# Kernel optimization log

Measured on AMD Instinct MI355X. Metric: run time of the kernel, lower is better.

The kernel has to match this reference:

```python
import jax, jax.numpy as jnp
import numpy as np

NEG = -1e30


def setup_inputs() -> dict:
    B, Lc, Lq, D = 64, 2048, 256, 128
    key = jax.random.key(0)
    kC, kQ, kcm, kqm, k1, k2, k3 = jax.random.split(key, 7)
    C = jax.random.normal(kC, (B, Lc, D), dtype=jnp.float32)
    Q = jax.random.normal(kQ, (B, Lq, D), dtype=jnp.float32)
    Cmask = jax.random.randint(kcm, (B, Lc), 0, 2).astype(jnp.float32)
    Qmask = jax.random.randint(kqm, (B, Lq), 0, 2).astype(jnp.float32)
    # xavier_uniform for (D,1): bound = sqrt(6/(D+1))
    b1 = float(np.sqrt(6.0 / (D + 1)))
    w4C = jax.random.uniform(k1, (D, 1), minval=-b1, maxval=b1, dtype=jnp.float32)
    w4Q = jax.random.uniform(k2, (D, 1), minval=-b1, maxval=b1, dtype=jnp.float32)
    # xavier_uniform for (1,1,D): fan_in=D, fan_out=1 on last two dims -> bound = sqrt(6/(1+D))
    w4mlu = jax.random.uniform(k3, (1, 1, D), minval=-b1, maxval=b1, dtype=jnp.float32)
    bias = jnp.zeros((1,), dtype=jnp.float32)
    return {"C": C, "Q": Q, "Cmask": Cmask, "Qmask": Qmask,
            "w4C": w4C, "w4Q": w4Q, "w4mlu": w4mlu, "bias": bias}


def reference(C, Q, Cmask, Qmask, w4C, w4Q, w4mlu, bias):
    # trilinear score S: [B, Lc, Lq]  (eval mode: dropout is identity)
    sub0 = C @ w4C                                   # [B, Lc, 1]
    sub1 = jnp.transpose(Q @ w4Q, (0, 2, 1))         # [B, 1, Lq]
    sub2 = jnp.einsum('bcd,bqd->bcq', C * w4mlu, Q)  # [B, Lc, Lq]
    S = sub0 + sub1 + sub2 + bias
    Qm = Qmask[:, None, :]   # [B, 1, Lq]
    Cm = Cmask[:, :, None]   # [B, Lc, 1]
    S1 = jax.nn.softmax(S + NEG * (1.0 - Qm), axis=2)  # over query
    S2 = jax.nn.softmax(S + NEG * (1.0 - Cm), axis=1)  # over context
    A = jnp.einsum('bcq,bqd->bcd', S1, Q)              # [B, Lc, D]
    Bt = jnp.einsum('bcq,bkq,bkd->bcd', S1, S2, C)     # S1 @ S2^T @ C
    out = jnp.concatenate([C, A, C * A, C * Bt], axis=2)  # [B, Lc, 4D]
    return jnp.transpose(out, (0, 2, 1))               # [B, 4D, Lc]
```

## Files before the change

### kernel.cpp

```cpp
#include <hip/hip_runtime.h>

#define B_ 64
#define LC 2048
#define LQ 256
#define DD 128

typedef __bf16 bf16;
typedef __bf16 bf16x8 __attribute__((ext_vector_type(8)));
typedef __bf16 bf16x4 __attribute__((ext_vector_type(4)));
typedef float f32x4 __attribute__((ext_vector_type(4)));

#define MFMA16(a, b, c) __builtin_amdgcn_mfma_f32_16x16x32_bf16((a), (b), (c), 0, 0, 0)


__global__ __launch_bounds__(256) void k_prep(const float* __restrict__ C,
    const float* __restrict__ Q, const float* __restrict__ w4C,
    const float* __restrict__ w4Q, const float* __restrict__ w4mlu,
    bf16* __restrict__ Cwp, bf16* __restrict__ CbTp,
    bf16* __restrict__ Qbp, bf16* __restrict__ QbTp,
    float* __restrict__ sub0, float* __restrict__ sub1, float* __restrict__ out)
{
    __shared__ float lds[64][DD + 4];
    int t = threadIdx.x;
    if (blockIdx.x < 2048) {
        int b = blockIdx.x >> 5, ct = blockIdx.x & 31;
        int c0 = ct * 64;
        int r = t >> 2, cb = (t & 3) * 32;
        size_t rowoff = ((size_t)(b * LC + c0 + r)) * DD + cb;
        const float4* src = (const float4*)(C + rowoff);
        float s0 = 0.f;
#pragma unroll
        for (int i = 0; i < 8; ++i) {
            float4 v = src[i];
            int d = cb + i * 4;
            lds[r][d] = v.x; lds[r][d + 1] = v.y; lds[r][d + 2] = v.z; lds[r][d + 3] = v.w;
            s0 += v.x * w4C[d] + v.y * w4C[d + 1] + v.z * w4C[d + 2] + v.w * w4C[d + 3];
        }
        s0 += __shfl_xor(s0, 1);
        s0 += __shfl_xor(s0, 2);
        if ((t & 3) == 0) sub0[b * LC + c0 + r] = s0;
        __syncthreads();

#pragma unroll
        for (int p = 0; p < 4; ++p) {
            int idx = p * 256 + t;
            int chunk = idx >> 6, w = idx & 63;
            int cb_l = chunk >> 2, ks = chunk & 3;
            int lr = w & 15, lg = w >> 4;
            int c_l = cb_l * 16 + lr, d0 = ks * 32 + lg * 8;
            bf16x8 v;
#pragma unroll
            for (int j = 0; j < 8; ++j) v[j] = (bf16)(lds[c_l][d0 + j] * w4mlu[d0 + j]);
            size_t off = ((size_t)((b * 128 + ct * 4 + cb_l) * 4 + ks)) * 512 + w * 8;
            *(bf16x8*)(Cwp + off) = v;
        }
#pragma unroll
        for (int p = 0; p < 4; ++p) {
            int idx = p * 256 + t;
            int cb32 = idx >> 9, rem = idx & 511;
            int d = rem >> 2, lg = rem & 3;
            int cl0 = cb32 * 32 + lg * 8;
            bf16x8 v;
#pragma unroll
            for (int j = 0; j < 8; ++j) v[j] = (bf16)lds[cl0 + j][d];
            size_t off = ((size_t)((b * 64 + ct * 2 + cb32) * 128 + d)) * 32 + lg * 8;
            *(bf16x8*)(CbTp + off) = v;
        }
#pragma unroll
        for (int p = 0; p < 8; ++p) {
            int d = p * 16 + (t >> 4);
            int cl = (t & 15) * 4;
            f32x4 v = {lds[cl][d], lds[cl + 1][d], lds[cl + 2][d], lds[cl + 3][d]};
            __builtin_nontemporal_store(v,
                (f32x4*)(out + ((size_t)(b * 512 + d)) * LC + c0 + cl));
        }
    } else {
        int idx0 = blockIdx.x - 2048;
        int b = idx0 >> 2, qt = idx0 & 3;
        int q0 = qt * 64;
        bf16* ldsb = (bf16*)lds;
        int r = t >> 2, cb = (t & 3) * 32;
        size_t rowoff = ((size_t)(b * LQ + q0 + r)) * DD + cb;
        const float4* src = (const float4*)(Q + rowoff);
        float s1 = 0.f;
#pragma unroll
        for (int i = 0; i < 8; ++i) {
            float4 v = src[i];
            int d = cb + i * 4;
            ldsb[r * 132 + d] = (bf16)v.x; ldsb[r * 132 + d + 1] = (bf16)v.y;
            ldsb[r * 132 + d + 2] = (bf16)v.z; ldsb[r * 132 + d + 3] = (bf16)v.w;
            s1 += v.x * w4Q[d] + v.y * w4Q[d + 1] + v.z * w4Q[d + 2] + v.w * w4Q[d + 3];
        }
        s1 += __shfl_xor(s1, 1);
        s1 += __shfl_xor(s1, 2);
        if ((t & 3) == 0) sub1[b * LQ + q0 + r] = s1;
        __syncthreads();

#pragma unroll
        for (int p = 0; p < 4; ++p) {
            int idx = p * 256 + t;
            int chunk = idx >> 6, w = idx & 63;
            int qb_l = chunk >> 2, ks = chunk & 3;
            int lr = w & 15, lg = w >> 4;
            bf16x8 v = *(bf16x8*)&ldsb[(qb_l * 16 + lr) * 132 + ks * 32 + lg * 8];
            size_t off = ((size_t)((b * 16 + qt * 4 + qb_l) * 4 + ks)) * 512 + w * 8;
            *(bf16x8*)(Qbp + off) = v;
        }
#pragma unroll
        for (int p = 0; p < 4; ++p) {
            int idx = p * 256 + t;
            int chunk = idx >> 6, w = idx & 63;
            int ks_l = chunk >> 3, dt = chunk & 7;
            int lr = w & 15, lg = w >> 4;
            int d = dt * 16 + lr, ql = ks_l * 32 + lg * 8;
            bf16x8 v;
#pragma unroll
            for (int j = 0; j < 8; ++j) v[j] = ldsb[(ql + j) * 132 + d];
            size_t off = ((size_t)((b * 8 + qt * 2 + ks_l) * 8 + dt)) * 512 + w * 8;
            *(bf16x8*)(QbTp + off) = v;
        }
    }
}

__global__ __launch_bounds__(256) void k_s(const bf16* __restrict__ Cwp,
    const bf16* __restrict__ Qbp, const float* __restrict__ sub0,
    const float* __restrict__ sub1, const float* __restrict__ Qmask,
    const float* __restrict__ Cmask, const float* __restrict__ bias,
    bf16* __restrict__ Pp, float* __restrict__ Rpart, float* __restrict__ Lpart)
{
    __shared__ bf16 ldsP[128][82];
    int id = blockIdx.x;
    int xcd = id & 7, slot = id >> 3;
    int b = xcd * 8 + (slot >> 6);
    int rem = slot & 63;
    int ctile = rem >> 2, qt = rem & 3;
    int q0 = qt * 64;
    int t = threadIdx.x, wid = t >> 6, lane = t & 63;
    int lr = lane & 15, lg = lane >> 4;
    int rowbase = ctile * 128 + wid * 32;

    f32x4 acc[2][4];
#pragma unroll
    for (int rt = 0; rt < 2; ++rt)
#pragma unroll
        for (int ct = 0; ct < 4; ++ct) acc[rt][ct] = (f32x4){0.f, 0.f, 0.f, 0.f};

    const bf16* Ab = Cwp + ((size_t)((b * 128 + ctile * 8 + wid * 2) * 4)) * 512 + lane * 8;
    const bf16* Bb = Qbp + ((size_t)((b * 16 + qt * 4) * 4)) * 512 + lane * 8;
#pragma unroll
    for (int ks = 0; ks < 4; ++ks) {
        bf16x8 a0 = *(const bf16x8*)(Ab + (size_t)ks * 512);
        bf16x8 a1 = *(const bf16x8*)(Ab + (size_t)(4 + ks) * 512);
#pragma unroll
        for (int ct = 0; ct < 4; ++ct) {
            bf16x8 bb = *(const bf16x8*)(Bb + (size_t)(ct * 4 + ks) * 512);
            acc[0][ct] = MFMA16(a0, bb, acc[0][ct]);
            acc[1][ct] = MFMA16(a1, bb, acc[1][ct]);
        }
    }

    float biasv = bias[0];
    float sub0v[2][4], cmv[2][4];
#pragma unroll
    for (int rt = 0; rt < 2; ++rt)
#pragma unroll
        for (int j = 0; j < 4; ++j) {
            int idx = b * LC + rowbase + rt * 16 + lg * 4 + j;
            sub0v[rt][j] = sub0[idx];
            cmv[rt][j] = Cmask[idx];
        }

    float rsum[2][4] = {};
#pragma unroll
    for (int ct = 0; ct < 4; ++ct) {
        int q = q0 + ct * 16 + lr;
        float s1v = sub1[b * LQ + q] + biasv;
        float qm = Qmask[b * LQ + q];
        float colsum = 0.f;
#pragma unroll
        for (int rt = 0; rt < 2; ++rt)
#pragma unroll
            for (int j = 0; j < 4; ++j) {
                float S = acc[rt][ct][j] + sub0v[rt][j] + s1v;
                float Pv = __expf(S - 8.0f) * qm;
                rsum[rt][j] += Pv;
                colsum += Pv * cmv[rt][j];
                ldsP[wid * 32 + rt * 16 + lg * 4 + j][ct * 16 + lr] = (bf16)Pv;
            }
        colsum += __shfl_xor(colsum, 16);
        colsum += __shfl_xor(colsum, 32);
        if (lg == 0)
            Lpart[((size_t)(b * 64 + ctile * 4 + wid)) * LQ + q] = colsum;
    }
#pragma unroll
    for (int rt = 0; rt < 2; ++rt)
#pragma unroll
        for (int j = 0; j < 4; ++j) {
            float s = rsum[rt][j];
            s += __shfl_xor(s, 1);
            s += __shfl_xor(s, 2);
            s += __shfl_xor(s, 4);
            s += __shfl_xor(s, 8);
            if (lr == 0)
                Rpart[((size_t)(b * 4 + qt)) * LC + rowbase + rt * 16 + lg * 4 + j] = s;
        }
    __syncthreads();

#pragma unroll
    for (int p = 0; p < 4; ++p) {
        int idx = p * 256 + t;
        int chunk = idx >> 6, w = idx & 63;
        int cb_l = chunk >> 1, ks_l = chunk & 1;
        int plr = w & 15, plg = w >> 4;
        bf16x8 v = *(bf16x8*)&ldsP[cb_l * 16 + plr][ks_l * 32 + plg * 8];
        size_t off = ((size_t)((b * 128 + ctile * 8 + cb_l) * 8 + qt * 2 + ks_l)) * 512 + w * 8;
        *(bf16x8*)(Pp + off) = v;
    }
}

__global__ __launch_bounds__(256) void k_m(const bf16* __restrict__ CbTp,
    const bf16* __restrict__ Pp, const float* __restrict__ Cmask,
    bf16* __restrict__ MTp)
{
    __shared__ bf16 stage[2][64 * 40];
    int id = blockIdx.x;
    int xcd = id & 7, slot = id >> 3;
    int b = xcd * 8 + (slot >> 4);
    int rem = slot & 15;
    int qt = rem & 3, ksl = rem >> 2;
    int t = threadIdx.x, wid = t >> 6, lane = t & 63;
    int lr = lane & 15, lg = lane >> 4;
    int dbase = wid * 32;

    f32x4 acc[2][4];
#pragma unroll
    for (int rt = 0; rt < 2; ++rt)
#pragma unroll
        for (int ct = 0; ct < 4; ++ct) acc[rt][ct] = (f32x4){0.f, 0.f, 0.f, 0.f};

    const bf16* Ab = CbTp + ((size_t)(b * 64 + ksl * 16) * 128 + dbase + lr) * 32 + lg * 8;
    const float* Mb = Cmask + b * LC + ksl * 512 + lg * 8;
    int cb_off = wid & 1, qh = wid >> 1;
    const bf16* Bsrc = Pp + ((size_t)((b * 128 + ksl * 32 + cb_off) * 8) + qt * 2 + qh) * 512
                       + lane * 8;
    int c_local = cb_off * 16 + lr;
    int qrow = qh * 32 + lg * 8;

    {
        bf16x8 g = *(const bf16x8*)Bsrc;
#pragma unroll
        for (int i = 0; i < 8; ++i) stage[0][(qrow + i) * 40 + c_local] = g[i];
    }
    __syncthreads();

    for (int ks = 0; ks < 16; ++ks) {
        int cur = ks & 1;
        bf16x8 g;
        if (ks < 15) g = *(const bf16x8*)(Bsrc + (size_t)(ks + 1) * 8192);
        bf16x8 a0 = *(const bf16x8*)(Ab + (size_t)ks * 4096);
        bf16x8 a1 = *(const bf16x8*)(Ab + (size_t)ks * 4096 + 512);
        f32x4 m0 = *(const f32x4*)(Mb + ks * 32);
        f32x4 m1 = *(const f32x4*)(Mb + ks * 32 + 4);
        bf16x8 msk;
#pragma unroll
        for (int i = 0; i < 4; ++i) { msk[i] = (bf16)m0[i]; msk[4 + i] = (bf16)m1[i]; }
        a0 = a0 * msk;
        a1 = a1 * msk;
#pragma unroll
        for (int ct = 0; ct < 4; ++ct) {
            bf16x8 bb = *(bf16x8*)&stage[cur][(ct * 16 + lr) * 40 + lg * 8];
            acc[0][ct] = MFMA16(a0, bb, acc[0][ct]);
            acc[1][ct] = MFMA16(a1, bb, acc[1][ct]);
        }
        if (ks < 15) {
#pragma unroll
            for (int i = 0; i < 8; ++i) stage[cur ^ 1][(qrow + i) * 40 + c_local] = g[i];
        }
        __syncthreads();
    }

    size_t base = ((((size_t)ksl * B_ + b) * 4 + qt) * 4 + wid) * 2048;
#pragma unroll
    for (int rt = 0; rt < 2; ++rt)
#pragma unroll
        for (int ct = 0; ct < 4; ++ct)
#pragma unroll
            for (int j = 0; j < 4; ++j)
                MTp[base + (size_t)(rt * 16 + ct * 4 + j) * 64 + lane] = (bf16)acc[rt][ct][j];
}

__global__ __launch_bounds__(256) void k_m2(const bf16* __restrict__ MTp,
    const float* __restrict__ Lpart, bf16* __restrict__ MTpn)
{
    __shared__ float ldsLinv[256];
    int b = blockIdx.y, ih = blockIdx.x;
    int t = threadIdx.x;
    {
        float s = 0.f;
#pragma unroll
        for (int sl = 0; sl < 64; ++sl) s += Lpart[((size_t)(b * 64 + sl)) * LQ + t];
        ldsLinv[t] = 1.0f / fmaxf(s, 1e-30f);
    }
    __syncthreads();
#pragma unroll
    for (int i = 0; i < 4; ++i) {
        int slot = (ih * 4 + i) * 256 + t;
        int d = slot >> 5, qo = slot & 31;
        int q0 = qo * 8;
        int qt = q0 >> 6, ct = (q0 >> 4) & 3, lr0 = q0 & 15;
        int wid = d >> 5, rt = (d >> 4) & 1, lgd = (d >> 2) & 3, j = d & 3;
        size_t roff = ((size_t)(b * 4 + qt)) * 8192 + wid * 2048
                      + (rt * 16 + ct * 4 + j) * 64 + lgd * 16 + lr0;
        float a8[8] = {0.f, 0.f, 0.f, 0.f, 0.f, 0.f, 0.f, 0.f};
#pragma unroll
        for (int sl = 0; sl < 4; ++sl) {
            bf16x8 x = *(const bf16x8*)(MTp + (size_t)sl * B_ * 32768 + roff);
#pragma unroll
            for (int k = 0; k < 8; ++k) a8[k] += (float)x[k];
        }
        bf16x8 o;
#pragma unroll
        for (int k = 0; k < 8; ++k) o[k] = (bf16)(a8[k] * ldsLinv[q0 + k]);
        size_t woff = ((size_t)((b * 8 + (qo >> 2)) * 8 + (d >> 4))) * 512
                      + ((qo & 3) * 16 + (d & 15)) * 8;
        *(bf16x8*)(MTpn + woff) = o;
    }
}

__global__ __launch_bounds__(256) void k_out(const bf16* __restrict__ Pp,
    const bf16* __restrict__ QbTp, const bf16* __restrict__ MTpn,
    const bf16* __restrict__ CbTp, const float* __restrict__ Rpart,
    float* __restrict__ out)
{
    __shared__ f32x4 smem4[2304];
    bf16* stage = (bf16*)smem4;
    bf16 (*ldsA)[72] = (bf16(*)[72])smem4;
    bf16 (*ldsB)[72] = (bf16(*)[72])((char*)smem4 + 18432);

    int id = blockIdx.x;
    int xcd = id & 7, slot = id >> 3;
    int b = xcd * 8 + (slot >> 5);
    int ctile = slot & 31;
    int t = threadIdx.x, wid = t >> 6, lane = t & 63;
    int lr = lane & 15, lg = lane >> 4;
    int c0 = ctile * 64;

    const bf16* gsrc = (wid < 2 ? QbTp : MTpn) + (size_t)b * 32768
                       + (size_t)(wid & 1) * 2048 + lane * 8;
    int ldst = wid * 2048 + lane * 8;

    f32x4 rs = (f32x4){0.f, 0.f, 0.f, 0.f};
#pragma unroll
    for (int s = 0; s < 4; ++s)
        rs += *(const f32x4*)(Rpart + ((size_t)(b * 4 + s)) * LC + c0 + wid * 16 + lg * 4);
    f32x4 rv;
#pragma unroll
    for (int j = 0; j < 4; ++j) rv[j] = 1.0f / fmaxf(rs[j], 1e-30f);

    f32x4 accA[8], accB[8];
#pragma unroll
    for (int dt = 0; dt < 8; ++dt) {
        accA[dt] = (f32x4){0.f, 0.f, 0.f, 0.f};
        accB[dt] = (f32x4){0.f, 0.f, 0.f, 0.f};
    }
    const bf16* Ab = Pp + ((size_t)((b * 128 + ctile * 4 + wid) * 8)) * 512 + lane * 8;

    {
        bf16x8 g0 = *(const bf16x8*)(gsrc);
        bf16x8 g1 = *(const bf16x8*)(gsrc + 512);
        bf16x8 g2 = *(const bf16x8*)(gsrc + 1024);
        bf16x8 g3 = *(const bf16x8*)(gsrc + 1536);
        *(bf16x8*)&stage[ldst]        = g0;
        *(bf16x8*)&stage[ldst + 512]  = g1;
        *(bf16x8*)&stage[ldst + 1024] = g2;
        *(bf16x8*)&stage[ldst + 1536] = g3;
    }
    __syncthreads();

    for (int ks = 0; ks < 8; ++ks) {
        int cur = (ks & 1) * 8192;
        bf16x8 g0, g1, g2, g3;
        if (ks < 7) {
            const bf16* gs = gsrc + (size_t)(ks + 1) * 4096;
            g0 = *(const bf16x8*)(gs);
            g1 = *(const bf16x8*)(gs + 512);
            g2 = *(const bf16x8*)(gs + 1024);
            g3 = *(const bf16x8*)(gs + 1536);
        }
        bf16x8 a = *(const bf16x8*)(Ab + (size_t)ks * 512);
        int foff = cur + lane * 8;
#pragma unroll
        for (int dt = 0; dt < 8; ++dt) {
            bf16x8 bq = *(bf16x8*)&stage[foff + dt * 512];
            bf16x8 bm = *(bf16x8*)&stage[foff + 4096 + dt * 512];
            accA[dt] = MFMA16(a, bq, accA[dt]);
            accB[dt] = MFMA16(a, bm, accB[dt]);
        }
        if (ks < 7) {
            int nb = cur ^ 8192;
            *(bf16x8*)&stage[nb + ldst]        = g0;
            *(bf16x8*)&stage[nb + ldst + 512]  = g1;
            *(bf16x8*)&stage[nb + ldst + 1024] = g2;
            *(bf16x8*)&stage[nb + ldst + 1536] = g3;
        }
        __syncthreads();
    }

    int fsub = t >> 4;
    int cq = (t & 15) * 4;
    int cglob = c0 + cq;
    int cb32g = cglob >> 5, cig = cglob & 31;
    bf16x4 cpre[8];
#pragma unroll
    for (int pass = 0; pass < 8; ++pass) {
        int d = pass * 16 + fsub;
        cpre[pass] = *(const bf16x4*)(CbTp + ((size_t)(b * 64 + cb32g) * 128 + d) * 32 + cig);
    }

#pragma unroll
    for (int dt = 0; dt < 8; ++dt) {
        f32x4 a4 = accA[dt] * rv;
        f32x4 b4 = accB[dt] * rv;
        bf16x4 pa = { (bf16)a4[0], (bf16)a4[1], (bf16)a4[2], (bf16)a4[3] };
        bf16x4 pb = { (bf16)b4[0], (bf16)b4[1], (bf16)b4[2], (bf16)b4[3] };
        *(bf16x4*)&ldsA[dt * 16 + lr][wid * 16 + lg * 4] = pa;
        *(bf16x4*)&ldsB[dt * 16 + lr][wid * 16 + lg * 4] = pb;
    }
    __syncthreads();

    float* obase = out + ((size_t)b * 512) * LC;
#pragma unroll
    for (int pass = 0; pass < 8; ++pass) {
        int d = pass * 16 + fsub;
        bf16x4 av = *(bf16x4*)&ldsA[d][cq];
        bf16x4 bv = *(bf16x4*)&ldsB[d][cq];
        bf16x4 cb4 = cpre[pass];
        f32x4 c4 = {(float)cb4[0], (float)cb4[1], (float)cb4[2], (float)cb4[3]};
        f32x4 a4 = {(float)av[0], (float)av[1], (float)av[2], (float)av[3]};
        f32x4 b4 = {(float)bv[0], (float)bv[1], (float)bv[2], (float)bv[3]};
        __builtin_nontemporal_store(a4, (f32x4*)(obase + (size_t)(128 + d) * LC + c0 + cq));
        __builtin_nontemporal_store(c4 * a4, (f32x4*)(obase + (size_t)(256 + d) * LC + c0 + cq));
        __builtin_nontemporal_store(c4 * b4, (f32x4*)(obase + (size_t)(384 + d) * LC + c0 + cq));
    }
}

extern "C" void kernel_launch(void* const* d_in, const int* in_sizes, int n_in,
                              void* d_out, int out_size, void* d_ws, size_t ws_size,
                              hipStream_t stream)
{
    const float* C     = (const float*)d_in[0];
    const float* Q     = (const float*)d_in[1];
    const float* Cmask = (const float*)d_in[2];
    const float* Qmask = (const float*)d_in[3];
    const float* w4C   = (const float*)d_in[4];
    const float* w4Q   = (const float*)d_in[5];
    const float* w4mlu = (const float*)d_in[6];
    const float* bias  = (const float*)d_in[7];
    float* out = (float*)d_out;

    char* ws = (char*)d_ws;
    size_t off = 0;
    auto alloc = [&](size_t bytes) -> char* {
        char* p = ws + off;
        off += (bytes + 255) & ~(size_t)255;
        return p;
    };
    bf16* Cwp   = (bf16*)alloc((size_t)B_ * LC * DD * 2);
    bf16* CbTp  = (bf16*)alloc((size_t)B_ * LC * DD * 2);
    bf16* Qbp   = (bf16*)alloc((size_t)B_ * LQ * DD * 2);
    bf16* QbTp  = (bf16*)alloc((size_t)B_ * LQ * DD * 2);
    bf16* Pp    = (bf16*)alloc((size_t)B_ * LC * LQ * 2);
    bf16* MTp   = (bf16*)alloc((size_t)4 * B_ * DD * LQ * 2);
    bf16* MTpn  = (bf16*)alloc((size_t)B_ * DD * LQ * 2);
    float* sub0 = (float*)alloc((size_t)B_ * LC * 4);
    float* sub1 = (float*)alloc((size_t)B_ * LQ * 4);
    float* Rpart = (float*)alloc((size_t)B_ * 4 * LC * 4);
    float* Lpart = (float*)alloc((size_t)B_ * 64 * LQ * 4);
    (void)ws_size; (void)in_sizes; (void)n_in; (void)out_size;

    hipLaunchKernelGGL(k_prep, dim3(2304), dim3(256), 0, stream,
                       C, Q, w4C, w4Q, w4mlu, Cwp, CbTp, Qbp, QbTp, sub0, sub1, out);
    hipLaunchKernelGGL(k_s, dim3(4096), dim3(256), 0, stream,
                       Cwp, Qbp, sub0, sub1, Qmask, Cmask, bias, Pp, Rpart, Lpart);
    hipLaunchKernelGGL(k_m, dim3(1024), dim3(256), 0, stream, CbTp, Pp, Cmask, MTp);
    hipLaunchKernelGGL(k_m2, dim3(4, B_), dim3(256), 0, stream, MTp, Lpart, MTpn);
    hipLaunchKernelGGL(k_out, dim3(2048), dim3(256), 0, stream,
                       Pp, QbTp, MTpn, CbTp, Rpart, out);
}
```

Baseline: 156.3 us.

## Fuse score/softmax kernel with masked C^T·P accumulation kernel

Merges k_s and k_m into a single k_sm kernel. Each block walks four 128-row context tiles, computes the score tile and exponentials, and writes P to global for later use. It also stages a transposed copy of P in shared memory and feeds it straight into the C^T·P MFMA accumulation, so P is no longer read back from global and one launch disappears. The cost is a smaller grid (1024 blocks instead of 4096), more shared memory per block and serialized stages inside each block, which may reduce parallelism and latency hiding.

```diff
diff --git a/kernel.cpp b/kernel.cpp
--- a/kernel.cpp
+++ b/kernel.cpp
@@ -122,161 +122,147 @@
     }
 }
 
-__global__ __launch_bounds__(256) void k_s(const bf16* __restrict__ Cwp,
-    const bf16* __restrict__ Qbp, const float* __restrict__ sub0,
-    const float* __restrict__ sub1, const float* __restrict__ Qmask,
-    const float* __restrict__ Cmask, const float* __restrict__ bias,
-    bf16* __restrict__ Pp, float* __restrict__ Rpart, float* __restrict__ Lpart)
+__global__ __launch_bounds__(256) void k_sm(const bf16* __restrict__ Cwp,
+    const bf16* __restrict__ Qbp, const bf16* __restrict__ CbTp,
+    const float* __restrict__ sub0, const float* __restrict__ sub1,
+    const float* __restrict__ Qmask, const float* __restrict__ Cmask,
+    const float* __restrict__ bias,
+    bf16* __restrict__ Pp, float* __restrict__ Rpart, float* __restrict__ Lpart,
+    bf16* __restrict__ MTp)
 {
     __shared__ bf16 ldsP[128][82];
-    int id = blockIdx.x;
-    int xcd = id & 7, slot = id >> 3;
-    int b = xcd * 8 + (slot >> 6);
-    int rem = slot & 63;
-    int ctile = rem >> 2, qt = rem & 3;
-    int q0 = qt * 64;
-    int t = threadIdx.x, wid = t >> 6, lane = t & 63;
-    int lr = lane & 15, lg = lane >> 4;
-    int rowbase = ctile * 128 + wid * 32;
-
-    f32x4 acc[2][4];
-#pragma unroll
-    for (int rt = 0; rt < 2; ++rt)
-#pragma unroll
-        for (int ct = 0; ct < 4; ++ct) acc[rt][ct] = (f32x4){0.f, 0.f, 0.f, 0.f};
-
-    const bf16* Ab = Cwp + ((size_t)((b * 128 + ctile * 8 + wid * 2) * 4)) * 512 + lane * 8;
-    const bf16* Bb = Qbp + ((size_t)((b * 16 + qt * 4) * 4)) * 512 + lane * 8;
-#pragma unroll
-    for (int ks = 0; ks < 4; ++ks) {
-        bf16x8 a0 = *(const bf16x8*)(Ab + (size_t)ks * 512);
-        bf16x8 a1 = *(const bf16x8*)(Ab + (size_t)(4 + ks) * 512);
-#pragma unroll
-        for (int ct = 0; ct < 4; ++ct) {
-            bf16x8 bb = *(const bf16x8*)(Bb + (size_t)(ct * 4 + ks) * 512);
-            acc[0][ct] = MFMA16(a0, bb, acc[0][ct]);
-            acc[1][ct] = MFMA16(a1, bb, acc[1][ct]);
-        }
-    }
-
-    float biasv = bias[0];
-    float sub0v[2][4], cmv[2][4];
-#pragma unroll
-    for (int rt = 0; rt < 2; ++rt)
-#pragma unroll
-        for (int j = 0; j < 4; ++j) {
-            int idx = b * LC + rowbase + rt * 16 + lg * 4 + j;
-            sub0v[rt][j] = sub0[idx];
-            cmv[rt][j] = Cmask[idx];
-        }
-
-    float rsum[2][4] = {};
-#pragma unroll
-    for (int ct = 0; ct < 4; ++ct) {
-        int q = q0 + ct * 16 + lr;
-        float s1v = sub1[b * LQ + q] + biasv;
-        float qm = Qmask[b * LQ + q];
-        float colsum = 0.f;
-#pragma unroll
-        for (int rt = 0; rt < 2; ++rt)
-#pragma unroll
-            for (int j = 0; j < 4; ++j) {
-                float S = acc[rt][ct][j] + sub0v[rt][j] + s1v;
-                float Pv = __expf(S - 8.0f) * qm;
-                rsum[rt][j] += Pv;
-                colsum += Pv * cmv[rt][j];
-                ldsP[wid * 32 + rt * 16 + lg * 4 + j][ct * 16 + lr] = (bf16)Pv;
-            }
-        colsum += __shfl_xor(colsum, 16);
-        colsum += __shfl_xor(colsum, 32);
-        if (lg == 0)
-            Lpart[((size_t)(b * 64 + ctile * 4 + wid)) * LQ + q] = colsum;
-    }
-#pragma unroll
-    for (int rt = 0; rt < 2; ++rt)
-#pragma unroll
-        for (int j = 0; j < 4; ++j) {
-            float s = rsum[rt][j];
-            s += __shfl_xor(s, 1);
-            s += __shfl_xor(s, 2);
-            s += __shfl_xor(s, 4);
-            s += __shfl_xor(s, 8);
-            if (lr == 0)
-                Rpart[((size_t)(b * 4 + qt)) * LC + rowbase + rt * 16 + lg * 4 + j] = s;
-        }
-    __syncthreads();
-
-#pragma unroll
-    for (int p = 0; p < 4; ++p) {
-        int idx = p * 256 + t;
-        int chunk = idx >> 6, w = idx & 63;
-        int cb_l = chunk >> 1, ks_l = chunk & 1;
-        int plr = w & 15, plg = w >> 4;
-        bf16x8 v = *(bf16x8*)&ldsP[cb_l * 16 + plr][ks_l * 32 + plg * 8];
-        size_t off = ((size_t)((b * 128 + ctile * 8 + cb_l) * 8 + qt * 2 + ks_l)) * 512 + w * 8;
-        *(bf16x8*)(Pp + off) = v;
-    }
-}
-
-__global__ __launch_bounds__(256) void k_m(const bf16* __restrict__ CbTp,
-    const bf16* __restrict__ Pp, const float* __restrict__ Cmask,
-    bf16* __restrict__ MTp)
-{
-    __shared__ bf16 stage[2][64 * 40];
+    __shared__ bf16 ldsPT[64][136];
     int id = blockIdx.x;
     int xcd = id & 7, slot = id >> 3;
     int b = xcd * 8 + (slot >> 4);
     int rem = slot & 15;
     int qt = rem & 3, ksl = rem >> 2;
+    int q0 = qt * 64;
     int t = threadIdx.x, wid = t >> 6, lane = t & 63;
     int lr = lane & 15, lg = lane >> 4;
     int dbase = wid * 32;
 
-    f32x4 acc[2][4];
+    float biasv = bias[0];
+    float s1v[4], qmv[4];
+#pragma unroll
+    for (int ct = 0; ct < 4; ++ct) {
+        int q = q0 + ct * 16 + lr;
+        s1v[ct] = sub1[b * LQ + q] + biasv;
+        qmv[ct] = Qmask[b * LQ + q];
+    }
+
+    f32x4 accM[2][4];
 #pragma unroll
     for (int rt = 0; rt < 2; ++rt)
 #pragma unroll
-        for (int ct = 0; ct < 4; ++ct) acc[rt][ct] = (f32x4){0.f, 0.f, 0.f, 0.f};
-
-    const bf16* Ab = CbTp + ((size_t)(b * 64 + ksl * 16) * 128 + dbase + lr) * 32 + lg * 8;
+        for (int ct = 0; ct < 4; ++ct) accM[rt][ct] = (f32x4){0.f, 0.f, 0.f, 0.f};
+
+    const bf16* Am_base = CbTp + ((size_t)(b * 64 + ksl * 16) * 128 + dbase + lr) * 32 + lg * 8;
     const float* Mb = Cmask + b * LC + ksl * 512 + lg * 8;
-    int cb_off = wid & 1, qh = wid >> 1;
-    const bf16* Bsrc = Pp + ((size_t)((b * 128 + ksl * 32 + cb_off) * 8) + qt * 2 + qh) * 512
-                       + lane * 8;
-    int c_local = cb_off * 16 + lr;
-    int qrow = qh * 32 + lg * 8;
-
-    {
-        bf16x8 g = *(const bf16x8*)Bsrc;
-#pragma unroll
-        for (int i = 0; i < 8; ++i) stage[0][(qrow + i) * 40 + c_local] = g[i];
-    }
-    __syncthreads();
-
-    for (int ks = 0; ks < 16; ++ks) {
-        int cur = ks & 1;
-        bf16x8 g;
-        if (ks < 15) g = *(const bf16x8*)(Bsrc + (size_t)(ks + 1) * 8192);
-        bf16x8 a0 = *(const bf16x8*)(Ab + (size_t)ks * 4096);
-        bf16x8 a1 = *(const bf16x8*)(Ab + (size_t)ks * 4096 + 512);
-        f32x4 m0 = *(const f32x4*)(Mb + ks * 32);
-        f32x4 m1 = *(const f32x4*)(Mb + ks * 32 + 4);
-        bf16x8 msk;
-#pragma unroll
-        for (int i = 0; i < 4; ++i) { msk[i] = (bf16)m0[i]; msk[4 + i] = (bf16)m1[i]; }
-        a0 = a0 * msk;
-        a1 = a1 * msk;
+    const bf16* Bb = Qbp + ((size_t)((b * 16 + qt * 4) * 4)) * 512 + lane * 8;
+
+    for (int st = 0; st < 4; ++st) {
+        int ctile = ksl * 4 + st;
+        int rowbase = ctile * 128 + wid * 32;
+
+        f32x4 acc[2][4];
+#pragma unroll
+        for (int rt = 0; rt < 2; ++rt)
+#pragma unroll
+            for (int ct = 0; ct < 4; ++ct) acc[rt][ct] = (f32x4){0.f, 0.f, 0.f, 0.f};
+        const bf16* Ab = Cwp + ((size_t)((b * 128 + ctile * 8 + wid * 2) * 4)) * 512 + lane * 8;
+#pragma unroll
+        for (int ks = 0; ks < 4; ++ks) {
+            bf16x8 a0 = *(const bf16x8*)(Ab + (size_t)ks * 512);
+            bf16x8 a1 = *(const bf16x8*)(Ab + (size_t)(4 + ks) * 512);
+#pragma unroll
+            for (int ct = 0; ct < 4; ++ct) {
+                bf16x8 bb = *(const bf16x8*)(Bb + (size_t)(ct * 4 + ks) * 512);
+                acc[0][ct] = MFMA16(a0, bb, acc[0][ct]);
+                acc[1][ct] = MFMA16(a1, bb, acc[1][ct]);
+            }
+        }
+
+        float sub0v[2][4], cmv[2][4];
+#pragma unroll
+        for (int rt = 0; rt < 2; ++rt)
+#pragma unroll
+            for (int j = 0; j < 4; ++j) {
+                int idx = b * LC + rowbase + rt * 16 + lg * 4 + j;
+                sub0v[rt][j] = sub0[idx];
+                cmv[rt][j] = Cmask[idx];
+            }
+
+        __syncthreads();
+
+        float rsum[2][4] = {};
 #pragma unroll
         for (int ct = 0; ct < 4; ++ct) {
-            bf16x8 bb = *(bf16x8*)&stage[cur][(ct * 16 + lr) * 40 + lg * 8];
-            acc[0][ct] = MFMA16(a0, bb, acc[0][ct]);
-            acc[1][ct] = MFMA16(a1, bb, acc[1][ct]);
-        }
-        if (ks < 15) {
-#pragma unroll
-            for (int i = 0; i < 8; ++i) stage[cur ^ 1][(qrow + i) * 40 + c_local] = g[i];
-        }
+            float colsum = 0.f;
+#pragma unroll
+            for (int rt = 0; rt < 2; ++rt) {
+                bf16x4 ptv;
+#pragma unroll
+                for (int j = 0; j < 4; ++j) {
+                    float S = acc[rt][ct][j] + sub0v[rt][j] + s1v[ct];
+                    float Pv = __expf(S - 8.0f) * qmv[ct];
+                    rsum[rt][j] += Pv;
+                    colsum += Pv * cmv[rt][j];
+                    bf16 pb = (bf16)Pv;
+                    ldsP[wid * 32 + rt * 16 + lg * 4 + j][ct * 16 + lr] = pb;
+                    ptv[j] = pb;
+                }
+                *(bf16x4*)&ldsPT[ct * 16 + lr][wid * 32 + rt * 16 + lg * 4] = ptv;
+            }
+            colsum += __shfl_xor(colsum, 16);
+            colsum += __shfl_xor(colsum, 32);
+            if (lg == 0)
+                Lpart[((size_t)(b * 64 + ctile * 4 + wid)) * LQ + q0 + ct * 16 + lr] = colsum;
+        }
+#pragma unroll
+        for (int rt = 0; rt < 2; ++rt)
+#pragma unroll
+            for (int j = 0; j < 4; ++j) {
+                float s = rsum[rt][j];
+                s += __shfl_xor(s, 1);
+                s += __shfl_xor(s, 2);
+                s += __shfl_xor(s, 4);
+                s += __shfl_xor(s, 8);
+                if (lr == 0)
+                    Rpart[((size_t)(b * 4 + qt)) * LC + rowbase + rt * 16 + lg * 4 + j] = s;
+            }
         __syncthreads();
+
+#pragma unroll
+        for (int p = 0; p < 4; ++p) {
+            int idx = p * 256 + t;
+            int chunk = idx >> 6, w = idx & 63;
+            int cb_l = chunk >> 1, ks_l = chunk & 1;
+            int plr = w & 15, plg = w >> 4;
+            bf16x8 v = *(bf16x8*)&ldsP[cb_l * 16 + plr][ks_l * 32 + plg * 8];
+            size_t off = ((size_t)((b * 128 + ctile * 8 + cb_l) * 8 + qt * 2 + ks_l)) * 512 + w * 8;
+            *(bf16x8*)(Pp + off) = v;
+        }
+
+#pragma unroll
+        for (int kf = 0; kf < 4; ++kf) {
+            int ks = st * 4 + kf;
+            bf16x8 a0 = *(const bf16x8*)(Am_base + (size_t)ks * 4096);
+            bf16x8 a1 = *(const bf16x8*)(Am_base + (size_t)ks * 4096 + 512);
+            f32x4 m0 = *(const f32x4*)(Mb + ks * 32);
+            f32x4 m1 = *(const f32x4*)(Mb + ks * 32 + 4);
+            bf16x8 msk;
+#pragma unroll
+            for (int i = 0; i < 4; ++i) { msk[i] = (bf16)m0[i]; msk[4 + i] = (bf16)m1[i]; }
+            a0 = a0 * msk;
+            a1 = a1 * msk;
+#pragma unroll
+            for (int ct = 0; ct < 4; ++ct) {
+                bf16x8 bb = *(bf16x8*)&ldsPT[ct * 16 + lr][kf * 32 + lg * 8];
+                accM[0][ct] = MFMA16(a0, bb, accM[0][ct]);
+                accM[1][ct] = MFMA16(a1, bb, accM[1][ct]);
+            }
+        }
     }
 
     size_t base = ((((size_t)ksl * B_ + b) * 4 + qt) * 4 + wid) * 2048;
@@ -286,7 +272,7 @@
         for (int ct = 0; ct < 4; ++ct)
 #pragma unroll
             for (int j = 0; j < 4; ++j)
-                MTp[base + (size_t)(rt * 16 + ct * 4 + j) * 64 + lane] = (bf16)acc[rt][ct][j];
+                MTp[base + (size_t)(rt * 16 + ct * 4 + j) * 64 + lane] = (bf16)accM[rt][ct][j];
 }
 
 __global__ __launch_bounds__(256) void k_m2(const bf16* __restrict__ MTp,
@@ -480,9 +466,9 @@
 
     hipLaunchKernelGGL(k_prep, dim3(2304), dim3(256), 0, stream,
                        C, Q, w4C, w4Q, w4mlu, Cwp, CbTp, Qbp, QbTp, sub0, sub1, out);
-    hipLaunchKernelGGL(k_s, dim3(4096), dim3(256), 0, stream,
-                       Cwp, Qbp, sub0, sub1, Qmask, Cmask, bias, Pp, Rpart, Lpart);
-    hipLaunchKernelGGL(k_m, dim3(1024), dim3(256), 0, stream, CbTp, Pp, Cmask, MTp);
+    hipLaunchKernelGGL(k_sm, dim3(1024), dim3(256), 0, stream,
+                       Cwp, Qbp, CbTp, sub0, sub1, Qmask, Cmask, bias,
+                       Pp, Rpart, Lpart, MTp);
     hipLaunchKernelGGL(k_m2, dim3(4, B_), dim3(256), 0, stream, MTp, Lpart, MTpn);
     hipLaunchKernelGGL(k_out, dim3(2048), dim3(256), 0, stream,
                        Pp, QbTp, MTpn, CbTp, Rpart, out);
```

New measurement: 150.2 us. 3.9% less time.
